# Optimization experiments

Measured on AMD Instinct MI355X. Metric: run time of the kernel, lower is better.

The kernel has to match this reference:

```python
import jax, jax.numpy as jnp
import numpy as np

SPACE_TOKEN = 63
STRIDE = 2
B, F, T, W = 16, 512, 8192, 4096


def setup_inputs() -> dict:
    key = jax.random.key(0)
    k1, k2, k3 = jax.random.split(key, 3)
    word_preds = jax.random.normal(k1, (B, F, W), dtype=jnp.float32)
    char_features = jax.random.normal(k2, (B, F, T), dtype=jnp.float32)
    target_chars = jax.random.randint(k3, (B, T), 0, 64, dtype=jnp.int32)
    return {"word_preds": word_preds, "char_features": char_features, "target_chars": target_chars}


def _per_batch(wp, cf, ch):
    # wp: (F, W) predicted word vectors; cf: (F, T) char features; ch: (T,) char ids
    Tn = ch.shape[0]
    Wn = wp.shape[1]
    space = ch == SPACE_TOKEN
    cum = jnp.cumsum(space.astype(jnp.int32))  # spaces seen up to and including t
    n_spaces = cum[-1]
    # span k lives strictly between space #k and space #(k+1) (0-indexed spaces).
    # a non-space char at t (with cum[t] spaces before it) belongs to span cum[t]-1.
    seg = jnp.where(space | (cum == 0), Tn, cum - 1)  # invalid chars -> dump segment Tn
    counts = jax.ops.segment_sum(jnp.ones((Tn,), jnp.int32), seg, num_segments=Tn + 1)[:Tn]
    sums = jax.ops.segment_sum(cf.T, seg, num_segments=Tn + 1)[:Tn]  # (Tn, F)
    # position of space #k via one-hot scatter of positions
    sid = jnp.where(space, cum - 1, Tn)
    pos_k = jax.ops.segment_sum(jnp.arange(Tn, dtype=jnp.int32), sid, num_segments=Tn + 1)[:Tn]
    word_pos = pos_k // STRIDE
    k = jnp.arange(Tn, dtype=jnp.int32)
    # valid span: a following space exists, span non-empty, word_pos in range
    valid = (k < n_spaces - 1) & (counts > 0) & (word_pos < Wn)
    target = sums / jnp.maximum(counts, 1).astype(sums.dtype)[:, None]  # span mean (detached in torch)
    target = jax.lax.stop_gradient(target)
    pred = wp[:, jnp.clip(word_pos, 0, Wn - 1)].T  # (Tn, F) gather of predictions
    mse = jnp.mean((pred - target) ** 2, axis=1)  # per-span mean over feat dim (F.mse_loss)
    return jnp.sum(jnp.where(valid, mse, 0.0)), jnp.sum(valid.astype(jnp.int32))


def reference(word_preds, char_features, target_chars):
    losses, cnts = jax.vmap(_per_batch)(word_preds, char_features, target_chars)
    total = jnp.sum(losses)
    count = jnp.sum(cnts)
    return jnp.where(count > 0, total / jnp.maximum(count, 1).astype(total.dtype), jnp.float32(0.0))
```

## Files before the change

kernel.cpp:

```cpp
#include <hip/hip_runtime.h>


constexpr int SPACE_TOKEN = 63;
constexpr int B = 16;
constexpr int FDIM = 512;
constexpr int T = 8192;
constexpr int W = 4096;
constexpr int ROWS = 8;
constexpr int NBLK = B * FDIM / ROWS;
constexpr int SENT = T;

__device__ __forceinline__ int swz(int u) { return u ^ ((u >> 3) & 7); }

#define BAR_VM8() do { asm volatile("s_waitcnt vmcnt(8)" ::: "memory"); \
  __builtin_amdgcn_s_barrier(); asm volatile("" ::: "memory"); } while (0)
#define BAR_VM0() do { asm volatile("s_waitcnt vmcnt(0)" ::: "memory"); \
  __builtin_amdgcn_s_barrier(); asm volatile("" ::: "memory"); } while (0)
#define BAR_LGKM() do { asm volatile("s_waitcnt lgkmcnt(0)" ::: "memory"); \
  __builtin_amdgcn_s_barrier(); asm volatile("" ::: "memory"); } while (0)

__device__ __forceinline__ void stage_row(const float4* __restrict__ src,
                                          float* dst, int tid, int wid) {
  float4* d4 = (float4*)dst;
  #pragma unroll
  for (int i = 0; i < 8; ++i) {
    const int u = i * 256 + tid;
    const float4* gsrc = src + swz(u);
    float4* ldst = d4 + (i * 256 + wid * 64);
    __builtin_amdgcn_global_load_lds(
        (const __attribute__((address_space(1))) void*)(const void*)gsrc,
        (__attribute__((address_space(3))) void*)(void*)ldst, 16, 0, 0);
  }
}

__global__ __launch_bounds__(256) void k_fused(
    const float* __restrict__ wp, const float* __restrict__ cf,
    const int* __restrict__ chars, float* __restrict__ partials,
    int* __restrict__ batchValid) {
  const int blk = blockIdx.x;
  const int row0 = blk * ROWS;
  const int b = row0 >> 9;
  __shared__ alignas(16) float buf[2][T];
  __shared__ alignas(16) float csum[256];
  __shared__ alignas(16) float cexc[256];
  __shared__ int posL[260];
  __shared__ int s_wtot[4], s_wpair[4];
  __shared__ float s_red[4];
  const int tid = threadIdx.x;
  const int lane = tid & 63;
  const int wid = tid >> 6;
  const int* cb = chars + (size_t)b * T;

  int4 creg[8];
  const int4* c4 = (const int4*)cb;
  #pragma unroll
  for (int i = 0; i < 8; ++i) creg[i] = c4[i * 256 + tid];

  stage_row((const float4*)(cf + (size_t)row0 * T), buf[0], tid, wid);

  asm volatile("s_waitcnt vmcnt(8)" ::: "memory");

  int4* b1 = (int4*)buf[1];
  #pragma unroll
  for (int i = 0; i < 8; ++i) b1[swz(i * 256 + tid)] = creg[i];
  posL[tid] = SENT;
  if (tid == 0) { posL[256] = SENT; posL[257] = SENT; }
  BAR_LGKM();

  int ch[32];
  #pragma unroll
  for (int i = 0; i < 8; ++i) {
    const int4 q = b1[swz(tid * 8 + i)];
    ch[i * 4 + 0] = q.x; ch[i * 4 + 1] = q.y;
    ch[i * 4 + 2] = q.z; ch[i * 4 + 3] = q.w;
  }
  int nxt = SPACE_TOKEN + 1;
  if (tid < 255) nxt = b1[swz((tid + 1) * 8)].x;

  int cnt = 0, pairs = 0;
  #pragma unroll
  for (int i = 0; i < 32; ++i) cnt += (ch[i] == SPACE_TOKEN);
  #pragma unroll
  for (int i = 0; i < 31; ++i)
    pairs += (ch[i] == SPACE_TOKEN) && (ch[i + 1] == SPACE_TOKEN);
  pairs += (ch[31] == SPACE_TOKEN) && (nxt == SPACE_TOKEN);

  int inc = cnt, pr = pairs;
  #pragma unroll
  for (int o = 1; o < 64; o <<= 1) {
    const int n = __shfl_up(inc, o);
    if (lane >= o) inc += n;
  }
  #pragma unroll
  for (int o = 32; o > 0; o >>= 1) pr += __shfl_down(pr, o);
  if (lane == 63) s_wtot[wid] = inc;
  if (lane == 0) s_wpair[wid] = pr;
  BAR_LGKM();

  int wexc = 0;
  for (int w = 0; w < wid; ++w) wexc += s_wtot[w];
  const int S = s_wtot[0] + s_wtot[1] + s_wtot[2] + s_wtot[3];
  const int P = s_wpair[0] + s_wpair[1] + s_wpair[2] + s_wpair[3];
  int rk = wexc + inc - cnt;
  #pragma unroll
  for (int i = 0; i < 32; ++i)
    if (ch[i] == SPACE_TOKEN) { if (rk < 257) posL[rk] = tid * 32 + i; ++rk; }
  BAR_LGKM();

  if ((blk & 63) == 0 && tid == 0)
    batchValid[b] = (S > 1 ? S - 1 : 0) - P;

  const int p0r = posL[tid];
  const int p1r = posL[tid + 1];
  const int gidx = (p0r >> 1) & (W - 1);
  const float* wpb = wp + (size_t)row0 * W + gidx;
  const float wv0 = wpb[0 * W];
  const float wv1 = wpb[1 * W];
  const float wv2 = wpb[2 * W];
  const float wv3 = wpb[3 * W];
  const float wv4 = wpb[4 * W];
  const float wv5 = wpb[5 * W];
  const float wv6 = wpb[6 * W];
  const float wv7 = wpb[7 * W];

  float acc = 0.f;
  #pragma unroll 1
  for (int r = 0; r < ROWS; ++r) {
    if (r + 1 < ROWS)
      stage_row((const float4*)(cf + (size_t)(row0 + r + 1) * T),
                buf[(r + 1) & 1], tid, wid);
    if (r + 1 < ROWS) { BAR_VM8(); } else { BAR_VM0(); }

    float* rowf = buf[r & 1];
    float4* r4 = (float4*)rowf;

    float4 v[8];
    #pragma unroll
    for (int i = 0; i < 8; ++i) v[i] = r4[swz(tid * 8 + i)];
    float run = 0.f;
    #pragma unroll
    for (int i = 0; i < 8; ++i) {
      v[i].x = (run += v[i].x);
      v[i].y = (run += v[i].y);
      v[i].z = (run += v[i].z);
      v[i].w = (run += v[i].w);
    }
    #pragma unroll
    for (int i = 0; i < 8; ++i) r4[swz(tid * 8 + i)] = v[i];
    csum[tid] = run;
    BAR_LGKM();

    if (tid < 64) {
      const float4 sv = ((const float4*)csum)[tid];
      const float l1 = sv.x + sv.y;
      const float l2 = l1 + sv.z;
      const float tot = l2 + sv.w;
      float pinc = tot;
      #pragma unroll
      for (int o = 1; o < 64; o <<= 1) {
        const float n = __shfl_up(pinc, o);
        if (tid >= o) pinc += n;
      }
      const float exc = pinc - tot;
      ((float4*)cexc)[tid] = make_float4(exc, exc + sv.x, exc + l1, exc + l2);
    }
    BAR_LGKM();

    if (tid < S - 1) {
      const int scnt = p1r - p0r - 1;
      if (scnt > 0) {
        const int ta = p1r - 1;
        const float Pa = rowf[(swz(ta >> 2) << 2) | (ta & 3)] + cexc[ta >> 5];
        const float Pb = rowf[(swz(p0r >> 2) << 2) | (p0r & 3)] + cexc[p0r >> 5];
        const float mean = (Pa - Pb) / (float)scnt;
        const float wvr = (r == 0) ? wv0 : (r == 1) ? wv1 : (r == 2) ? wv2 :
                          (r == 3) ? wv3 : (r == 4) ? wv4 : (r == 5) ? wv5 :
                          (r == 6) ? wv6 : wv7;
        const float d = wvr - mean;
        acc += d * d;
      }
    }
    if (S - 1 > 256) {
      int want = 256 + tid;
      if (want < S - 1) {
        int rank2 = 0;
        int p0 = -1;
        for (int t = 0; t < T; ++t) {
          if (cb[t] == SPACE_TOKEN) {
            if (rank2 == want) {
              p0 = t;
            } else if (rank2 == want + 1) {
              const int scnt = t - p0 - 1;
              if (scnt > 0) {
                const int ta = t - 1;
                const float Pa = rowf[(swz(ta >> 2) << 2) | (ta & 3)] + cexc[ta >> 5];
                const float Pb = rowf[(swz(p0 >> 2) << 2) | (p0 & 3)] + cexc[p0 >> 5];
                const float mean = (Pa - Pb) / (float)scnt;
                const float d = wp[(size_t)(row0 + r) * W + (p0 >> 1)] - mean;
                acc += d * d;
              }
              want += 256;
              if (want >= S - 1) break;
            }
            rank2++;
          }
        }
      }
    }
    BAR_LGKM();
  }

  #pragma unroll
  for (int o = 32; o > 0; o >>= 1) acc += __shfl_down(acc, o);
  if (lane == 0) s_red[wid] = acc;
  __syncthreads();
  if (tid == 0) partials[blk] = s_red[0] + s_red[1] + s_red[2] + s_red[3];
}

__global__ __launch_bounds__(256) void k_finalize(
    const float* __restrict__ partials, const int* __restrict__ batchValid,
    float* __restrict__ out) {
  __shared__ float s_red[4];
  __shared__ int s_cnt[4];
  const int tid = threadIdx.x;
  const int lane = tid & 63;
  const int wid = tid >> 6;
  float s = 0.f;
  for (int i = tid; i < NBLK; i += 256) s += partials[i];
  int cnt = 0;
  for (int i = tid; i < B; i += 256) cnt += batchValid[i];
  for (int o = 32; o > 0; o >>= 1) {
    s += __shfl_down(s, o);
    cnt += __shfl_down(cnt, o);
  }
  if (lane == 0) { s_red[wid] = s; s_cnt[wid] = cnt; }
  __syncthreads();
  if (tid == 0) {
    const float total = s_red[0] + s_red[1] + s_red[2] + s_red[3];
    const int c = s_cnt[0] + s_cnt[1] + s_cnt[2] + s_cnt[3];
    out[0] = (c > 0) ? total / ((float)FDIM * (float)c) : 0.f;
  }
}

extern "C" void kernel_launch(void* const* d_in, const int* in_sizes, int n_in,
                              void* d_out, int out_size, void* d_ws, size_t ws_size,
                              hipStream_t stream) {
  const float* wp = (const float*)d_in[0];
  const float* cf = (const float*)d_in[1];
  const int* chars = (const int*)d_in[2];
  float* out = (float*)d_out;

  char* ws = (char*)d_ws;
  float* partials = (float*)ws;
  int* batchValid = (int*)(ws + NBLK * 4);

  k_fused<<<NBLK, 256, 0, stream>>>(wp, cf, chars, partials, batchValid);
  k_finalize<<<1, 256, 0, stream>>>(partials, batchValid, out);
}
```

Before: 72.47 us.

## Fuse finalize into main kernel via last-block atomic and read chars directly

Drops the separate finalize kernel: each block publishes its partial, bumps a global atomic counter, and the last block to finish does the final reduction and writes the output. A memset of the counter replaces the second launch. It also stops staging the character ids through LDS with a barrier, loading each thread's 32 contiguous chars plus its neighbour straight into registers. This saves one launch and one barrier, but adds a memset node, a threadfence and an atomic per block, and the contiguous per-thread char loads are less coalesced.

```diff
diff --git a/kernel.cpp b/kernel.cpp
--- a/kernel.cpp
+++ b/kernel.cpp
@@ -36,7 +36,8 @@
 __global__ __launch_bounds__(256) void k_fused(
     const float* __restrict__ wp, const float* __restrict__ cf,
     const int* __restrict__ chars, float* __restrict__ partials,
-    int* __restrict__ batchValid) {
+    int* __restrict__ batchValid, unsigned int* __restrict__ counter,
+    float* __restrict__ out) {
   const int blk = blockIdx.x;
   const int row0 = blk * ROWS;
   const int b = row0 >> 9;
@@ -46,45 +47,45 @@
   __shared__ int posL[260];
   __shared__ int s_wtot[4], s_wpair[4];
   __shared__ float s_red[4];
+  __shared__ int s_last;
+  __shared__ float f_red[4];
+  __shared__ int f_cnt[4];
   const int tid = threadIdx.x;
   const int lane = tid & 63;
   const int wid = tid >> 6;
   const int* cb = chars + (size_t)b * T;
 
-  int4 creg[8];
+  int4 ch4[8];
   const int4* c4 = (const int4*)cb;
   #pragma unroll
-  for (int i = 0; i < 8; ++i) creg[i] = c4[i * 256 + tid];
+  for (int i = 0; i < 8; ++i) ch4[i] = c4[tid * 8 + i];
+  const int nxtAddr = (tid < 255) ? (tid * 32 + 32) : (T - 1);
+  int nxt = cb[nxtAddr];
 
   stage_row((const float4*)(cf + (size_t)row0 * T), buf[0], tid, wid);
 
   asm volatile("s_waitcnt vmcnt(8)" ::: "memory");
-
-  int4* b1 = (int4*)buf[1];
-  #pragma unroll
-  for (int i = 0; i < 8; ++i) b1[swz(i * 256 + tid)] = creg[i];
+  if (tid == 255) nxt = SPACE_TOKEN + 1;
+
   posL[tid] = SENT;
-  if (tid == 0) { posL[256] = SENT; posL[257] = SENT; }
-  BAR_LGKM();
-
-  int ch[32];
-  #pragma unroll
-  for (int i = 0; i < 8; ++i) {
-    const int4 q = b1[swz(tid * 8 + i)];
-    ch[i * 4 + 0] = q.x; ch[i * 4 + 1] = q.y;
-    ch[i * 4 + 2] = q.z; ch[i * 4 + 3] = q.w;
-  }
-  int nxt = SPACE_TOKEN + 1;
-  if (tid < 255) nxt = b1[swz((tid + 1) * 8)].x;
+  if (tid == 0) { posL[256] = SENT; posL[257] = SENT; posL[258] = SENT; }
 
   int cnt = 0, pairs = 0;
-  #pragma unroll
-  for (int i = 0; i < 32; ++i) cnt += (ch[i] == SPACE_TOKEN);
-  #pragma unroll
-  for (int i = 0; i < 31; ++i)
-    pairs += (ch[i] == SPACE_TOKEN) && (ch[i + 1] == SPACE_TOKEN);
-  pairs += (ch[31] == SPACE_TOKEN) && (nxt == SPACE_TOKEN);
-
+  {
+    int last = SPACE_TOKEN + 1;
+    #pragma unroll
+    for (int i = 0; i < 8; ++i) {
+      const int4 q = ch4[i];
+      cnt += (q.x == SPACE_TOKEN) + (q.y == SPACE_TOKEN) +
+             (q.z == SPACE_TOKEN) + (q.w == SPACE_TOKEN);
+      pairs += (last == SPACE_TOKEN) && (q.x == SPACE_TOKEN);
+      pairs += (q.x == SPACE_TOKEN) && (q.y == SPACE_TOKEN);
+      pairs += (q.y == SPACE_TOKEN) && (q.z == SPACE_TOKEN);
+      pairs += (q.z == SPACE_TOKEN) && (q.w == SPACE_TOKEN);
+      last = q.w;
+    }
+    pairs += (last == SPACE_TOKEN) && (nxt == SPACE_TOKEN);
+  }
   int inc = cnt, pr = pairs;
   #pragma unroll
   for (int o = 1; o < 64; o <<= 1) {
@@ -103,12 +104,15 @@
   const int P = s_wpair[0] + s_wpair[1] + s_wpair[2] + s_wpair[3];
   int rk = wexc + inc - cnt;
   #pragma unroll
-  for (int i = 0; i < 32; ++i)
-    if (ch[i] == SPACE_TOKEN) { if (rk < 257) posL[rk] = tid * 32 + i; ++rk; }
+  for (int i = 0; i < 8; ++i) {
+    const int4 q = ch4[i];
+    const int t0 = tid * 32 + i * 4;
+    if (q.x == SPACE_TOKEN) { if (rk < 258) posL[rk] = t0 + 0; ++rk; }
+    if (q.y == SPACE_TOKEN) { if (rk < 258) posL[rk] = t0 + 1; ++rk; }
+    if (q.z == SPACE_TOKEN) { if (rk < 258) posL[rk] = t0 + 2; ++rk; }
+    if (q.w == SPACE_TOKEN) { if (rk < 258) posL[rk] = t0 + 3; ++rk; }
+  }
   BAR_LGKM();
-
-  if ((blk & 63) == 0 && tid == 0)
-    batchValid[b] = (S > 1 ? S - 1 : 0) - P;
 
   const int p0r = posL[tid];
   const int p1r = posL[tid + 1];
@@ -214,31 +218,31 @@
   for (int o = 32; o > 0; o >>= 1) acc += __shfl_down(acc, o);
   if (lane == 0) s_red[wid] = acc;
   __syncthreads();
-  if (tid == 0) partials[blk] = s_red[0] + s_red[1] + s_red[2] + s_red[3];
-}
-
-__global__ __launch_bounds__(256) void k_finalize(
-    const float* __restrict__ partials, const int* __restrict__ batchValid,
-    float* __restrict__ out) {
-  __shared__ float s_red[4];
-  __shared__ int s_cnt[4];
-  const int tid = threadIdx.x;
-  const int lane = tid & 63;
-  const int wid = tid >> 6;
-  float s = 0.f;
-  for (int i = tid; i < NBLK; i += 256) s += partials[i];
-  int cnt = 0;
-  for (int i = tid; i < B; i += 256) cnt += batchValid[i];
-  for (int o = 32; o > 0; o >>= 1) {
-    s += __shfl_down(s, o);
-    cnt += __shfl_down(cnt, o);
-  }
-  if (lane == 0) { s_red[wid] = s; s_cnt[wid] = cnt; }
+  if (tid == 0) {
+    partials[blk] = s_red[0] + s_red[1] + s_red[2] + s_red[3];
+    if ((blk & 63) == 0) batchValid[b] = (S > 1 ? S - 1 : 0) - P;
+    __threadfence();
+    const unsigned int old = atomicAdd(counter, 1u);
+    s_last = (old == (unsigned int)(NBLK - 1)) ? 1 : 0;
+  }
   __syncthreads();
-  if (tid == 0) {
-    const float total = s_red[0] + s_red[1] + s_red[2] + s_red[3];
-    const int c = s_cnt[0] + s_cnt[1] + s_cnt[2] + s_cnt[3];
-    out[0] = (c > 0) ? total / ((float)FDIM * (float)c) : 0.f;
+  if (s_last) {
+    __threadfence();
+    float s = 0.f;
+    for (int i = tid; i < NBLK; i += 256) s += partials[i];
+    int c2 = 0;
+    for (int i = tid; i < B; i += 256) c2 += batchValid[i];
+    for (int o = 32; o > 0; o >>= 1) {
+      s += __shfl_down(s, o);
+      c2 += __shfl_down(c2, o);
+    }
+    if (lane == 0) { f_red[wid] = s; f_cnt[wid] = c2; }
+    __syncthreads();
+    if (tid == 0) {
+      const float total = f_red[0] + f_red[1] + f_red[2] + f_red[3];
+      const int c = f_cnt[0] + f_cnt[1] + f_cnt[2] + f_cnt[3];
+      out[0] = (c > 0) ? total / ((float)FDIM * (float)c) : 0.f;
+    }
   }
 }
 
@@ -253,7 +257,9 @@
   char* ws = (char*)d_ws;
   float* partials = (float*)ws;
   int* batchValid = (int*)(ws + NBLK * 4);
-
-  k_fused<<<NBLK, 256, 0, stream>>>(wp, cf, chars, partials, batchValid);
-  k_finalize<<<1, 256, 0, stream>>>(partials, batchValid, out);
+  unsigned int* counter = (unsigned int*)(ws + NBLK * 4 + B * 4);
+
+  hipMemsetAsync(counter, 0, 4, stream);
+  k_fused<<<NBLK, 256, 0, stream>>>(wp, cf, chars, partials, batchValid,
+                                    counter, out);
 }
```

New measurement: 117.3 us. 1.62x slower.

## Split row staging into half-row LDS buffers to raise occupancy

Applied to the files above, without the earlier changes.

Replaces the two full-row (2x32KB) LDS buffers with two half-row buffers (2x16KB). Each row is scanned in two halves, with a carried prefix between them, and the next row's first half is prefetched while the second half is processed. Launch bounds request 4 blocks per CU, and the char load now reads contiguous per-thread chunks directly instead of bouncing them through LDS. This adds extra barriers and scan passes per row in exchange for higher occupancy, and the rare overflow path now sums spans directly from global memory.

```diff
diff --git a/kernel.cpp b/kernel.cpp
--- a/kernel.cpp
+++ b/kernel.cpp
@@ -8,22 +8,23 @@
 constexpr int W = 4096;
 constexpr int ROWS = 8;
 constexpr int NBLK = B * FDIM / ROWS;
+constexpr int HALF = 4096;
 constexpr int SENT = T;
 
 __device__ __forceinline__ int swz(int u) { return u ^ ((u >> 3) & 7); }
 
-#define BAR_VM8() do { asm volatile("s_waitcnt vmcnt(8)" ::: "memory"); \
+#define BAR_VM4() do { asm volatile("s_waitcnt vmcnt(4)" ::: "memory"); \
   __builtin_amdgcn_s_barrier(); asm volatile("" ::: "memory"); } while (0)
 #define BAR_VM0() do { asm volatile("s_waitcnt vmcnt(0)" ::: "memory"); \
   __builtin_amdgcn_s_barrier(); asm volatile("" ::: "memory"); } while (0)
 #define BAR_LGKM() do { asm volatile("s_waitcnt lgkmcnt(0)" ::: "memory"); \
   __builtin_amdgcn_s_barrier(); asm volatile("" ::: "memory"); } while (0)
 
-__device__ __forceinline__ void stage_row(const float4* __restrict__ src,
-                                          float* dst, int tid, int wid) {
+__device__ __forceinline__ void stage_half(const float4* __restrict__ src,
+                                           float* dst, int tid, int wid) {
   float4* d4 = (float4*)dst;
   #pragma unroll
-  for (int i = 0; i < 8; ++i) {
+  for (int i = 0; i < 4; ++i) {
     const int u = i * 256 + tid;
     const float4* gsrc = src + swz(u);
     float4* ldst = d4 + (i * 256 + wid * 64);
@@ -33,58 +34,57 @@
   }
 }
 
-__global__ __launch_bounds__(256) void k_fused(
+__global__ __launch_bounds__(256, 4) void k_fused(
     const float* __restrict__ wp, const float* __restrict__ cf,
     const int* __restrict__ chars, float* __restrict__ partials,
     int* __restrict__ batchValid) {
   const int blk = blockIdx.x;
   const int row0 = blk * ROWS;
   const int b = row0 >> 9;
-  __shared__ alignas(16) float buf[2][T];
+  __shared__ alignas(16) float buf0[HALF];
+  __shared__ alignas(16) float buf1[HALF];
   __shared__ alignas(16) float csum[256];
   __shared__ alignas(16) float cexc[256];
   __shared__ int posL[260];
   __shared__ int s_wtot[4], s_wpair[4];
   __shared__ float s_red[4];
+  __shared__ float s_carry;
   const int tid = threadIdx.x;
   const int lane = tid & 63;
   const int wid = tid >> 6;
   const int* cb = chars + (size_t)b * T;
 
-  int4 creg[8];
+  int4 ch4[8];
   const int4* c4 = (const int4*)cb;
   #pragma unroll
-  for (int i = 0; i < 8; ++i) creg[i] = c4[i * 256 + tid];
-
-  stage_row((const float4*)(cf + (size_t)row0 * T), buf[0], tid, wid);
-
-  asm volatile("s_waitcnt vmcnt(8)" ::: "memory");
-
-  int4* b1 = (int4*)buf[1];
-  #pragma unroll
-  for (int i = 0; i < 8; ++i) b1[swz(i * 256 + tid)] = creg[i];
+  for (int i = 0; i < 8; ++i) ch4[i] = c4[tid * 8 + i];
+  const int nxtAddr = (tid < 255) ? (tid * 32 + 32) : (T - 1);
+  int nxt = cb[nxtAddr];
+
+  stage_half((const float4*)(cf + (size_t)row0 * T), buf0, tid, wid);
+
+  asm volatile("s_waitcnt vmcnt(4)" ::: "memory");
+  if (tid == 255) nxt = SPACE_TOKEN + 1;
+
   posL[tid] = SENT;
-  if (tid == 0) { posL[256] = SENT; posL[257] = SENT; }
-  BAR_LGKM();
-
-  int ch[32];
-  #pragma unroll
-  for (int i = 0; i < 8; ++i) {
-    const int4 q = b1[swz(tid * 8 + i)];
-    ch[i * 4 + 0] = q.x; ch[i * 4 + 1] = q.y;
-    ch[i * 4 + 2] = q.z; ch[i * 4 + 3] = q.w;
-  }
-  int nxt = SPACE_TOKEN + 1;
-  if (tid < 255) nxt = b1[swz((tid + 1) * 8)].x;
+  if (tid == 0) { posL[256] = SENT; posL[257] = SENT; posL[258] = SENT; }
 
   int cnt = 0, pairs = 0;
-  #pragma unroll
-  for (int i = 0; i < 32; ++i) cnt += (ch[i] == SPACE_TOKEN);
-  #pragma unroll
-  for (int i = 0; i < 31; ++i)
-    pairs += (ch[i] == SPACE_TOKEN) && (ch[i + 1] == SPACE_TOKEN);
-  pairs += (ch[31] == SPACE_TOKEN) && (nxt == SPACE_TOKEN);
-
+  {
+    int last = SPACE_TOKEN + 1;
+    #pragma unroll
+    for (int i = 0; i < 8; ++i) {
+      const int4 q = ch4[i];
+      cnt += (q.x == SPACE_TOKEN) + (q.y == SPACE_TOKEN) +
+             (q.z == SPACE_TOKEN) + (q.w == SPACE_TOKEN);
+      pairs += (last == SPACE_TOKEN) && (q.x == SPACE_TOKEN);
+      pairs += (q.x == SPACE_TOKEN) && (q.y == SPACE_TOKEN);
+      pairs += (q.y == SPACE_TOKEN) && (q.z == SPACE_TOKEN);
+      pairs += (q.z == SPACE_TOKEN) && (q.w == SPACE_TOKEN);
+      last = q.w;
+    }
+    pairs += (last == SPACE_TOKEN) && (nxt == SPACE_TOKEN);
+  }
   int inc = cnt, pr = pairs;
   #pragma unroll
   for (int o = 1; o < 64; o <<= 1) {
@@ -103,8 +103,14 @@
   const int P = s_wpair[0] + s_wpair[1] + s_wpair[2] + s_wpair[3];
   int rk = wexc + inc - cnt;
   #pragma unroll
-  for (int i = 0; i < 32; ++i)
-    if (ch[i] == SPACE_TOKEN) { if (rk < 257) posL[rk] = tid * 32 + i; ++rk; }
+  for (int i = 0; i < 8; ++i) {
+    const int4 q = ch4[i];
+    const int t0 = tid * 32 + i * 4;
+    if (q.x == SPACE_TOKEN) { if (rk < 258) posL[rk] = t0 + 0; ++rk; }
+    if (q.y == SPACE_TOKEN) { if (rk < 258) posL[rk] = t0 + 1; ++rk; }
+    if (q.z == SPACE_TOKEN) { if (rk < 258) posL[rk] = t0 + 2; ++rk; }
+    if (q.w == SPACE_TOKEN) { if (rk < 258) posL[rk] = t0 + 3; ++rk; }
+  }
   BAR_LGKM();
 
   if ((blk & 63) == 0 && tid == 0)
@@ -123,33 +129,40 @@
   const float wv6 = wpb[6 * W];
   const float wv7 = wpb[7 * W];
 
-  float acc = 0.f;
+  const bool spanOk = (tid < S - 1) && (p1r - p0r - 1 > 0);
+  const int scnt = p1r - p0r - 1;
+  const int ta = p1r - 1;
+
+  float Pb_st = 0.f, rcarry = 0.f, acc = 0.f;
+
   #pragma unroll 1
   for (int r = 0; r < ROWS; ++r) {
-    if (r + 1 < ROWS)
-      stage_row((const float4*)(cf + (size_t)(row0 + r + 1) * T),
-                buf[(r + 1) & 1], tid, wid);
-    if (r + 1 < ROWS) { BAR_VM8(); } else { BAR_VM0(); }
-
-    float* rowf = buf[r & 1];
-    float4* r4 = (float4*)rowf;
-
-    float4 v[8];
-    #pragma unroll
-    for (int i = 0; i < 8; ++i) v[i] = r4[swz(tid * 8 + i)];
-    float run = 0.f;
-    #pragma unroll
-    for (int i = 0; i < 8; ++i) {
-      v[i].x = (run += v[i].x);
-      v[i].y = (run += v[i].y);
-      v[i].z = (run += v[i].z);
-      v[i].w = (run += v[i].w);
-    }
-    #pragma unroll
-    for (int i = 0; i < 8; ++i) r4[swz(tid * 8 + i)] = v[i];
-    csum[tid] = run;
-    BAR_LGKM();
-
+    const float wvr = (r == 0) ? wv0 : (r == 1) ? wv1 : (r == 2) ? wv2 :
+                      (r == 3) ? wv3 : (r == 4) ? wv4 : (r == 5) ? wv5 :
+                      (r == 6) ? wv6 : wv7;
+    const float* crow = cf + (size_t)(row0 + r) * T;
+
+    stage_half((const float4*)(crow + HALF), buf1, tid, wid);
+    BAR_VM4();
+
+    {
+      float4* r4 = (float4*)buf0;
+      float4 v[4];
+      #pragma unroll
+      for (int i = 0; i < 4; ++i) v[i] = r4[swz(tid * 4 + i)];
+      float run = 0.f;
+      #pragma unroll
+      for (int i = 0; i < 4; ++i) {
+        v[i].x = (run += v[i].x);
+        v[i].y = (run += v[i].y);
+        v[i].z = (run += v[i].z);
+        v[i].w = (run += v[i].w);
+      }
+      #pragma unroll
+      for (int i = 0; i < 4; ++i) r4[swz(tid * 4 + i)] = v[i];
+      csum[tid] = run;
+    }
+    BAR_LGKM();
     if (tid < 64) {
       const float4 sv = ((const float4*)csum)[tid];
       const float l1 = sv.x + sv.y;
@@ -163,22 +176,74 @@
       }
       const float exc = pinc - tot;
       ((float4*)cexc)[tid] = make_float4(exc, exc + sv.x, exc + l1, exc + l2);
-    }
-    BAR_LGKM();
-
-    if (tid < S - 1) {
-      const int scnt = p1r - p0r - 1;
-      if (scnt > 0) {
-        const int ta = p1r - 1;
-        const float Pa = rowf[(swz(ta >> 2) << 2) | (ta & 3)] + cexc[ta >> 5];
-        const float Pb = rowf[(swz(p0r >> 2) << 2) | (p0r & 3)] + cexc[p0r >> 5];
-        const float mean = (Pa - Pb) / (float)scnt;
-        const float wvr = (r == 0) ? wv0 : (r == 1) ? wv1 : (r == 2) ? wv2 :
-                          (r == 3) ? wv3 : (r == 4) ? wv4 : (r == 5) ? wv5 :
-                          (r == 6) ? wv6 : wv7;
+      if (tid == 63) s_carry = pinc;
+    }
+    BAR_LGKM();
+    rcarry = s_carry;
+    if (spanOk) {
+      if (p0r < HALF)
+        Pb_st = buf0[(swz(p0r >> 2) << 2) | (p0r & 3)] + cexc[p0r >> 4];
+      if (ta < HALF) {
+        const float Pa = buf0[(swz(ta >> 2) << 2) | (ta & 3)] + cexc[ta >> 4];
+        const float mean = (Pa - Pb_st) / (float)scnt;
         const float d = wvr - mean;
         acc += d * d;
       }
+    }
+    BAR_LGKM();
+
+    if (r + 1 < ROWS)
+      stage_half((const float4*)(cf + (size_t)(row0 + r + 1) * T), buf0,
+                 tid, wid);
+    if (r + 1 < ROWS) { BAR_VM4(); } else { BAR_VM0(); }
+
+    {
+      float4* r4 = (float4*)buf1;
+      float4 v[4];
+      #pragma unroll
+      for (int i = 0; i < 4; ++i) v[i] = r4[swz(tid * 4 + i)];
+      float run = 0.f;
+      #pragma unroll
+      for (int i = 0; i < 4; ++i) {
+        v[i].x = (run += v[i].x);
+        v[i].y = (run += v[i].y);
+        v[i].z = (run += v[i].z);
+        v[i].w = (run += v[i].w);
+      }
+      #pragma unroll
+      for (int i = 0; i < 4; ++i) r4[swz(tid * 4 + i)] = v[i];
+      csum[tid] = run;
+    }
+    BAR_LGKM();
+    if (tid < 64) {
+      const float4 sv = ((const float4*)csum)[tid];
+      const float l1 = sv.x + sv.y;
+      const float l2 = l1 + sv.z;
+      const float tot = l2 + sv.w;
+      float pinc = tot;
+      #pragma unroll
+      for (int o = 1; o < 64; o <<= 1) {
+        const float n = __shfl_up(pinc, o);
+        if (tid >= o) pinc += n;
+      }
+      const float exc = pinc - tot;
+      ((float4*)cexc)[tid] = make_float4(exc, exc + sv.x, exc + l1, exc + l2);
+    }
+    BAR_LGKM();
+    if (spanOk && ta >= HALF) {
+      const int tb = ta - HALF;
+      const float Pa = buf1[(swz(tb >> 2) << 2) | (tb & 3)] + cexc[tb >> 4]
+                       + rcarry;
+      float Pb;
+      if (p0r < HALF) {
+        Pb = Pb_st;
+      } else {
+        const int pb = p0r - HALF;
+        Pb = buf1[(swz(pb >> 2) << 2) | (pb & 3)] + cexc[pb >> 4] + rcarry;
+      }
+      const float mean = (Pa - Pb) / (float)scnt;
+      const float d = wvr - mean;
+      acc += d * d;
     }
     if (S - 1 > 256) {
       int want = 256 + tid;
@@ -190,12 +255,11 @@
             if (rank2 == want) {
               p0 = t;
             } else if (rank2 == want + 1) {
-              const int scnt = t - p0 - 1;
-              if (scnt > 0) {
-                const int ta = t - 1;
-                const float Pa = rowf[(swz(ta >> 2) << 2) | (ta & 3)] + cexc[ta >> 5];
-                const float Pb = rowf[(swz(p0 >> 2) << 2) | (p0 & 3)] + cexc[p0 >> 5];
-                const float mean = (Pa - Pb) / (float)scnt;
+              const int sc = t - p0 - 1;
+              if (sc > 0) {
+                float ssum = 0.f;
+                for (int u = p0 + 1; u < t; ++u) ssum += crow[u];
+                const float mean = ssum / (float)sc;
                 const float d = wp[(size_t)(row0 + r) * W + (p0 >> 1)] - mean;
                 acc += d * d;
               }
```

New measurement: 71.66 us. About the same (-1.1%).
